# Optimization experiments

Hardware: AMD Instinct MI355X
Metric: run time of the kernel (lower is better)

Reference implementation:

```python
import jax, jax.numpy as jnp
import numpy as np

M1, M2 = 20, 20  # retained DCT modes per layer

def dct1_last(x):
    # scipy.fftpack unnormalized DCT-I along last axis via FFT of even extension
    N = x.shape[-1]
    ext = jnp.concatenate([x, x[..., -2:0:-1]], axis=-1)  # length 2N-2
    return jnp.fft.rfft(ext).real[..., :N]

def dct1_2d(x):
    x = dct1_last(x)                       # along axis -1
    x = dct1_last(x.swapaxes(-1, -2)).swapaxes(-1, -2)  # along axis -2
    return x

def setup_inputs() -> dict:
    key = jax.random.key(0)
    ks = jax.random.split(key, 11)
    B, X, Y, Din, C, FC, Dout, L = 8, 256, 256, 3, 64, 128, 1, 3
    scale = 1.0 / (C * C)
    return {
        "x": jax.random.normal(ks[0], (B, X, Y, Din), jnp.float32),
        "fc0_w": jax.random.normal(ks[1], (Din, C), jnp.float32) * 0.1,
        "fc0_b": jax.random.normal(ks[2], (C,), jnp.float32) * 0.1,
        "sp_w1": scale * jax.random.uniform(ks[3], (L, C, C, M1, M2), jnp.float32),
        "sp_w2": scale * jax.random.uniform(ks[4], (L, C, C, M1, M2), jnp.float32),
        "conv_w": jax.random.normal(ks[5], (L, C, C), jnp.float32) * 0.05,
        "conv_b": jax.random.normal(ks[6], (L, C), jnp.float32) * 0.05,
        "fc1_w": jax.random.normal(ks[7], (C, FC), jnp.float32) * 0.05,
        "fc1_b": jax.random.normal(ks[8], (FC,), jnp.float32) * 0.05,
        "fc2_w": jax.random.normal(ks[9], (FC, Dout), jnp.float32) * 0.05,
        "fc2_b": jax.random.normal(ks[10], (Dout,), jnp.float32) * 0.05,
    }

def reference(x, fc0_w, fc0_b, sp_w1, sp_w2, conv_w, conv_b, fc1_w, fc1_b, fc2_w, fc2_b):
    h = x @ fc0_w + fc0_b                  # (B, X, Y, C)
    h = h.transpose(0, 3, 1, 2)            # (B, C, X, Y)
    B, C, X, Y = h.shape
    n_layers = sp_w1.shape[0]
    for i in range(n_layers):
        hd = dct1_2d(h)                    # forward DCT-I (unnormalized)
        # spectral mode multiply, scattered into zero spectrum (imag part is 0)
        out = jnp.zeros((B, C, X, Y), h.dtype)
        out = out.at[:, :, :M1, :M2].set(
            jnp.einsum('bixy,ioxy->boxy', hd[:, :, :M1, :M2], sp_w1[i]))
        out = out.at[:, :, X - M1:, :M2].set(
            jnp.einsum('bixy,ioxy->boxy', hd[:, :, X - M1:, :M2], sp_w2[i]))
        x1 = dct1_2d(out)                  # fftpack idct type-1 == dct type-1 (unnormalized)
        x2 = jnp.einsum('bixy,oi->boxy', h, conv_w[i]) + conv_b[i][None, :, None, None]
        h = x1 + x2
        if i != n_layers - 1:
            h = jnp.tanh(h)
    h = h.transpose(0, 2, 3, 1)            # (B, X, Y, C)
    h = jnp.tanh(h @ fc1_w + fc1_b)
    return h @ fc2_w + fc2_b               # (B, X, Y, 1)
```

## Files before the change

### kernel.cpp

```cpp
#include <hip/hip_runtime.h>
#include <math.h>

#define BB    8
#define CC    64
#define NN    256
#define MM    20
#define NKK   40
#define NLAY  3
#define FCD   128
#define PLANE (NN*NN)

__device__ __forceinline__ float fast_tanh(float x) {
    float xc = fminf(fmaxf(x, -15.f), 15.f);
    float e = __expf(2.f * xc);
    return (e - 1.f) / (e + 1.f);
}

__global__ __launch_bounds__(256) void k_basis(float* __restrict__ FlT, float* __restrict__ FkT,
                                               float* __restrict__ BkT, float* __restrict__ BlT,
                                               float* __restrict__ CwT, const float* __restrict__ conv_w) {
    int t = threadIdx.x;
    const double PI = 3.14159265358979323846;
    for (int j = t; j < NN*MM; j += 256) {
        int y = j / MM, l = j % MM;
        double g = (y == 0 || y == NN-1) ? 1.0 : 2.0;
        FlT[j] = (float)(g * cos(PI * (double)(l*y) / (double)(NN-1)));
    }
    for (int j = t; j < NN*NKK; j += 256) {
        int x = j / NKK, k = j % NKK;
        int rk = (k < MM) ? k : (NN - NKK + k);
        double g = (x == 0 || x == NN-1) ? 1.0 : 2.0;
        FkT[j] = (float)(g * cos(PI * (double)(rk*x) / (double)(NN-1)));
    }
    for (int j = t; j < NKK*NN; j += 256) {
        int k = j / NN, p = j % NN;
        int rk = (k < MM) ? k : (NN - NKK + k);
        double g = (rk == 0 || rk == NN-1) ? 1.0 : 2.0;
        BkT[j] = (float)(g * cos(PI * (double)(rk*p) / (double)(NN-1)));
    }
    for (int j = t; j < MM*NN; j += 256) {
        int l = j / NN, q = j % NN;
        double g = (l == 0) ? 1.0 : 2.0;
        BlT[j] = (float)(g * cos(PI * (double)(q*l) / (double)(NN-1)));
    }
    for (int j = t; j < NLAY*CC*CC; j += 256) {
        int lay = j / (CC*CC), r = j % (CC*CC);
        int i = r / CC, o = r % CC;
        CwT[j] = conv_w[lay*CC*CC + o*CC + i];
    }
}

__global__ __launch_bounds__(256) void k_fc0(const float* __restrict__ xin, const float* __restrict__ w,
                                             const float* __restrict__ bias, float* __restrict__ h) {
    __shared__ float xs[NN*3];
    int b = blockIdx.x >> 8, p = blockIdx.x & 255, q = threadIdx.x;
    size_t rowbase = ((size_t)(b*NN + p)*NN) * 3;
    for (int j = q; j < NN*3; j += 256) xs[j] = xin[rowbase + j];
    __syncthreads();
    float v0 = xs[q*3+0], v1 = xs[q*3+1], v2 = xs[q*3+2];
    size_t obase = (size_t)b*CC*PLANE + (size_t)p*NN + q;
    #pragma unroll 8
    for (int c = 0; c < CC; ++c) {
        float hv = bias[c] + v0*w[c] + v1*w[CC+c] + v2*w[2*CC+c];
        h[obase + (size_t)c*PLANE] = hv;
    }
}

__global__ __launch_bounds__(256, 4) void k_fwd(const float* __restrict__ h, const float* __restrict__ FkT,
                                                const float* __restrict__ FlT, float* __restrict__ Gt) {
    __shared__ float P[MM][NN+1];
    int plane = blockIdx.x >> 1;
    int g = blockIdx.x & 1;
    int t = threadIdx.x;
    const float* hp = h + (size_t)plane * PLANE;
    const float* fk = FkT + g*MM;
    float acc[MM];
    #pragma unroll
    for (int k = 0; k < MM; ++k) acc[k] = 0.f;
    #pragma unroll 4
    for (int x = 0; x < NN; ++x) {
        float hv = hp[x*NN + t];
        const float* fr = &fk[x*NKK];
        #pragma unroll
        for (int k = 0; k < MM; ++k) acc[k] += fr[k] * hv;
    }
    #pragma unroll
    for (int k = 0; k < MM; ++k) P[k][t] = acc[k];
    __syncthreads();
    int b = plane >> 6, c = plane & 63;
    for (int j = t; j < MM*MM; j += 256) {
        int kk = j / MM, l = j % MM;
        float a = 0.f;
        for (int y = 0; y < NN; ++y) a += P[kk][y] * FlT[y*MM + l];
        Gt[((size_t)((g*MM + kk)*BB + b)*CC + c)*MM + l] = a;
    }
}

__global__ __launch_bounds__(256, 2) void k_spec(const float* __restrict__ Gt, const float* __restrict__ w1,
                                                 const float* __restrict__ w2, float* __restrict__ S) {
    extern __shared__ float gl[];
    int kb = blockIdx.x;
    int t = threadIdx.x;
    const float* chunk = Gt + (size_t)kb * (BB*CC*MM);
    for (int j = t; j < BB*CC*MM; j += 256) gl[j] = chunk[j];
    __syncthreads();
    int o = t & 63, g = t >> 6;
    int b0 = 2*g, b1 = 2*g + 1;
    const float* wp; int kk;
    if (kb < MM) { wp = w1; kk = kb; } else { wp = w2; kk = kb - MM; }
    float a0[MM], a1[MM];
    #pragma unroll
    for (int l = 0; l < MM; ++l) { a0[l] = 0.f; a1[l] = 0.f; }
    for (int i = 0; i < CC; ++i) {
        const float4* wr4 = reinterpret_cast<const float4*>(wp + ((size_t)(i*CC + o)*MM + kk)*MM);
        const float4* g04 = reinterpret_cast<const float4*>(&gl[(b0*CC + i)*MM]);
        const float4* g14 = reinterpret_cast<const float4*>(&gl[(b1*CC + i)*MM]);
        #pragma unroll
        for (int l4 = 0; l4 < MM/4; ++l4) {
            float4 wv = wr4[l4];
            float4 gv0 = g04[l4];
            float4 gv1 = g14[l4];
            a0[4*l4+0] += wv.x*gv0.x; a0[4*l4+1] += wv.y*gv0.y;
            a0[4*l4+2] += wv.z*gv0.z; a0[4*l4+3] += wv.w*gv0.w;
            a1[4*l4+0] += wv.x*gv1.x; a1[4*l4+1] += wv.y*gv1.y;
            a1[4*l4+2] += wv.z*gv1.z; a1[4*l4+3] += wv.w*gv1.w;
        }
    }
    #pragma unroll
    for (int l = 0; l < MM; ++l) {
        S[((size_t)(b0*NKK + kb)*MM + l)*CC + o] = a0[l];
        S[((size_t)(b1*NKK + kb)*MM + l)*CC + o] = a1[l];
    }
}

__global__ __launch_bounds__(256, 2) void k_inv1(const float* __restrict__ S, const float* __restrict__ BkT,
                                                 float* __restrict__ U) {
    int b = blockIdx.x >> 8, p = blockIdx.x & 255;
    int o = threadIdx.x & 63, w = threadIdx.x >> 6;
    float acc[5];
    #pragma unroll
    for (int j = 0; j < 5; ++j) acc[j] = 0.f;
    for (int k = 0; k < NKK; ++k) {
        float bk = BkT[k*NN + p];
        const float* sb = S + ((size_t)(b*NKK + k)*MM + w)*CC + o;
        #pragma unroll
        for (int j = 0; j < 5; ++j) acc[j] += bk * sb[(size_t)(4*j)*CC];
    }
    float* ub = U + ((size_t)(b*NN + p)*MM + w)*CC + o;
    #pragma unroll
    for (int j = 0; j < 5; ++j) ub[(size_t)(4*j)*CC] = acc[j];
}

__global__ __launch_bounds__(256, 4) void k_combine(float* h, const float* __restrict__ U,
                                                    const float* __restrict__ BlT, const float* __restrict__ cwt,
                                                    const float* __restrict__ cb) {
    int qc = blockIdx.x & 3;
    int p  = (blockIdx.x >> 2) & 255;
    int b  = blockIdx.x >> 10;
    int lane = threadIdx.x & 63;
    int w = __builtin_amdgcn_readfirstlane(threadIdx.x >> 6);
    int q = qc*64 + lane;
    int o0 = w*16;
    float acc[16];
    #pragma unroll
    for (int oo = 0; oo < 16; ++oo) acc[oo] = cb[o0 + oo];
    float* hb = h + (size_t)b*CC*PLANE + (size_t)p*NN + q;
    #pragma unroll 4
    for (int i = 0; i < CC; ++i) {
        float hv = hb[(size_t)i*PLANE];
        const float* wr = &cwt[i*CC + o0];
        #pragma unroll
        for (int oo = 0; oo < 16; ++oo) acc[oo] += wr[oo]*hv;
    }
    const float* ub = U + ((size_t)(b*NN + p)*MM)*CC + o0;
    #pragma unroll 4
    for (int l = 0; l < MM; ++l) {
        float blv = BlT[l*NN + q];
        const float* ur = ub + (size_t)l*CC;
        #pragma unroll
        for (int oo = 0; oo < 16; ++oo) acc[oo] += ur[oo]*blv;
    }
    __syncthreads();
    #pragma unroll
    for (int oo = 0; oo < 16; ++oo) hb[(size_t)(o0 + oo)*PLANE] = fast_tanh(acc[oo]);
}

__global__ __launch_bounds__(256, 2) void k_combine_fc(const float* __restrict__ h, const float* __restrict__ U,
        const float* __restrict__ BlT, const float* __restrict__ cwt, const float* __restrict__ cb,
        const float* __restrict__ w1, const float* __restrict__ b1,
        const float* __restrict__ w2, const float* __restrict__ b2, float* __restrict__ out) {
    int b = blockIdx.x >> 8, p = blockIdx.x & 255;
    int q = threadIdx.x;
    float acc[CC];
    #pragma unroll
    for (int o = 0; o < CC; ++o) acc[o] = cb[o];
    const float* hb = h + (size_t)b*CC*PLANE + (size_t)p*NN + q;
    #pragma unroll 4
    for (int i = 0; i < CC; ++i) {
        float hv = hb[(size_t)i*PLANE];
        const float* wr = &cwt[i*CC];
        #pragma unroll
        for (int o = 0; o < CC; ++o) acc[o] += wr[o]*hv;
    }
    const float* ub = U + ((size_t)(b*NN + p)*MM)*CC;
    #pragma unroll 2
    for (int l = 0; l < MM; ++l) {
        float blv = BlT[l*NN + q];
        const float* ur = ub + (size_t)l*CC;
        #pragma unroll
        for (int o = 0; o < CC; ++o) acc[o] += ur[o]*blv;
    }
    float ov = b2[0];
    const int FCH = 8;
    for (int f0 = 0; f0 < FCD; f0 += FCH) {
        float a[FCH];
        #pragma unroll
        for (int f = 0; f < FCH; ++f) a[f] = b1[f0 + f];
        #pragma unroll
        for (int i = 0; i < CC; ++i) {
            float hv = acc[i];
            const float* wr = &w1[i*FCD + f0];
            #pragma unroll
            for (int f = 0; f < FCH; ++f) a[f] += hv*wr[f];
        }
        #pragma unroll
        for (int f = 0; f < FCH; ++f) ov += fast_tanh(a[f]) * w2[f0 + f];
    }
    out[(size_t)blockIdx.x*NN + q] = ov;
}

extern "C" void kernel_launch(void* const* d_in, const int* in_sizes, int n_in,
                              void* d_out, int out_size, void* d_ws, size_t ws_size,
                              hipStream_t stream) {
    const float* x      = (const float*)d_in[0];
    const float* fc0_w  = (const float*)d_in[1];
    const float* fc0_b  = (const float*)d_in[2];
    const float* sp_w1  = (const float*)d_in[3];
    const float* sp_w2  = (const float*)d_in[4];
    const float* conv_w = (const float*)d_in[5];
    const float* conv_b = (const float*)d_in[6];
    const float* fc1_w  = (const float*)d_in[7];
    const float* fc1_b  = (const float*)d_in[8];
    const float* fc2_w  = (const float*)d_in[9];
    const float* fc2_b  = (const float*)d_in[10];

    float* ws = (float*)d_ws;
    const size_t HSZ = (size_t)BB*CC*PLANE;
    float* hA  = ws;
    float* Gt  = hA + HSZ;
    float* S   = Gt + (size_t)NKK*BB*CC*MM;
    float* U   = S  + (size_t)BB*NKK*MM*CC;
    float* FlT = U  + (size_t)BB*NN*MM*CC;
    float* FkT = FlT + NN*MM;
    float* BkT = FkT + NN*NKK;
    float* BlT = BkT + NKK*NN;
    float* CwT = BlT + MM*NN;

    k_basis<<<1, 256, 0, stream>>>(FlT, FkT, BkT, BlT, CwT, conv_w);
    k_fc0<<<BB*NN, 256, 0, stream>>>(x, fc0_w, fc0_b, hA);

    for (int lay = 0; lay < NLAY; ++lay) {
        const float* w1 = sp_w1 + (size_t)lay*CC*CC*MM*MM;
        const float* w2 = sp_w2 + (size_t)lay*CC*CC*MM*MM;
        k_fwd<<<BB*CC*2, 256, 0, stream>>>(hA, FkT, FlT, Gt);
        k_spec<<<NKK, 256, BB*CC*MM*sizeof(float), stream>>>(Gt, w1, w2, S);
        k_inv1<<<BB*NN, 256, 0, stream>>>(S, BkT, U);
        if (lay != NLAY-1) {
            k_combine<<<BB*NN*4, 256, 0, stream>>>(
                hA, U, BlT, CwT + lay*CC*CC, conv_b + lay*CC);
        } else {
            k_combine_fc<<<BB*NN, 256, 0, stream>>>(
                hA, U, BlT, CwT + lay*CC*CC, conv_b + lay*CC,
                fc1_w, fc1_b, fc2_w, fc2_b, (float*)d_out);
        }
    }
}
```

Measured before the change: 993.3 us.

## Fuse inverse DCT row stage into combine kernel via shared memory

For the first two layers, the first inverse-transform stage (k_inv1) is folded into the combine kernel. Each block computes its row's 20x64 U slice into LDS and then does the 1x1 conv plus inverse column transform, with each thread now covering all 64 output channels. This removes the U round trip through global memory and one launch per layer. In exchange each block recomputes its U slice, the block count drops from 8192 to 2048, and 64 accumulators per thread raise register pressure and may lower occupancy.

```diff
diff --git a/kernel.cpp b/kernel.cpp
--- a/kernel.cpp
+++ b/kernel.cpp
@@ -151,38 +151,54 @@
     for (int j = 0; j < 5; ++j) ub[(size_t)(4*j)*CC] = acc[j];
 }
 
-__global__ __launch_bounds__(256, 4) void k_combine(float* h, const float* __restrict__ U,
-                                                    const float* __restrict__ BlT, const float* __restrict__ cwt,
-                                                    const float* __restrict__ cb) {
-    int qc = blockIdx.x & 3;
-    int p  = (blockIdx.x >> 2) & 255;
-    int b  = blockIdx.x >> 10;
-    int lane = threadIdx.x & 63;
-    int w = __builtin_amdgcn_readfirstlane(threadIdx.x >> 6);
-    int q = qc*64 + lane;
-    int o0 = w*16;
-    float acc[16];
-    #pragma unroll
-    for (int oo = 0; oo < 16; ++oo) acc[oo] = cb[o0 + oo];
+__global__ __launch_bounds__(256, 2) void k_combine_inv(float* h, const float* __restrict__ S,
+                                                        const float* __restrict__ BkT,
+                                                        const float* __restrict__ BlT,
+                                                        const float* __restrict__ cwt,
+                                                        const float* __restrict__ cb) {
+    __shared__ float ul[MM*CC];
+    int b = blockIdx.x >> 8, p = blockIdx.x & 255;
+    int t = threadIdx.x;
+    {
+        float s[5];
+        #pragma unroll
+        for (int j = 0; j < 5; ++j) s[j] = 0.f;
+        const float* sb = S + (size_t)b*NKK*MM*CC + t;
+        for (int k = 0; k < NKK; ++k) {
+            float bk = BkT[k*NN + p];
+            const float* sk = sb + (size_t)k*MM*CC;
+            #pragma unroll
+            for (int j = 0; j < 5; ++j) s[j] += bk * sk[j*256];
+        }
+        #pragma unroll
+        for (int j = 0; j < 5; ++j) ul[j*256 + t] = s[j];
+    }
+    __syncthreads();
+    int q = t;
+    float acc[CC];
+    #pragma unroll
+    for (int o = 0; o < CC; ++o) acc[o] = cb[o];
     float* hb = h + (size_t)b*CC*PLANE + (size_t)p*NN + q;
     #pragma unroll 4
     for (int i = 0; i < CC; ++i) {
         float hv = hb[(size_t)i*PLANE];
-        const float* wr = &cwt[i*CC + o0];
-        #pragma unroll
-        for (int oo = 0; oo < 16; ++oo) acc[oo] += wr[oo]*hv;
-    }
-    const float* ub = U + ((size_t)(b*NN + p)*MM)*CC + o0;
-    #pragma unroll 4
+        const float* wr = &cwt[i*CC];
+        #pragma unroll
+        for (int o = 0; o < CC; ++o) acc[o] += wr[o]*hv;
+    }
+    #pragma unroll 2
     for (int l = 0; l < MM; ++l) {
         float blv = BlT[l*NN + q];
-        const float* ur = ub + (size_t)l*CC;
-        #pragma unroll
-        for (int oo = 0; oo < 16; ++oo) acc[oo] += ur[oo]*blv;
-    }
-    __syncthreads();
-    #pragma unroll
-    for (int oo = 0; oo < 16; ++oo) hb[(size_t)(o0 + oo)*PLANE] = fast_tanh(acc[oo]);
+        const float4* u4 = reinterpret_cast<const float4*>(&ul[l*CC]);
+        #pragma unroll
+        for (int o4 = 0; o4 < CC/4; ++o4) {
+            float4 uv = u4[o4];
+            acc[4*o4+0] += uv.x*blv; acc[4*o4+1] += uv.y*blv;
+            acc[4*o4+2] += uv.z*blv; acc[4*o4+3] += uv.w*blv;
+        }
+    }
+    #pragma unroll
+    for (int o = 0; o < CC; ++o) hb[(size_t)o*PLANE] = fast_tanh(acc[o]);
 }
 
 __global__ __launch_bounds__(256, 2) void k_combine_fc(const float* __restrict__ h, const float* __restrict__ U,
@@ -264,11 +280,11 @@
         const float* w2 = sp_w2 + (size_t)lay*CC*CC*MM*MM;
         k_fwd<<<BB*CC*2, 256, 0, stream>>>(hA, FkT, FlT, Gt);
         k_spec<<<NKK, 256, BB*CC*MM*sizeof(float), stream>>>(Gt, w1, w2, S);
-        k_inv1<<<BB*NN, 256, 0, stream>>>(S, BkT, U);
         if (lay != NLAY-1) {
-            k_combine<<<BB*NN*4, 256, 0, stream>>>(
-                hA, U, BlT, CwT + lay*CC*CC, conv_b + lay*CC);
+            k_combine_inv<<<BB*NN, 256, 0, stream>>>(
+                hA, S, BkT, BlT, CwT + lay*CC*CC, conv_b + lay*CC);
         } else {
+            k_inv1<<<BB*NN, 256, 0, stream>>>(S, BkT, U);
             k_combine_fc<<<BB*NN, 256, 0, stream>>>(
                 hA, U, BlT, CwT + lay*CC*CC, conv_b + lay*CC,
                 fc1_w, fc1_b, fc2_w, fc2_b, (float*)d_out);
```

Result: slower. 1.034 ms (+4.1%).
